# Kernel optimization log

Measured on AMD Instinct MI355X. Metric: run time of the kernel, lower is better.

## Reference

```python
import jax, jax.numpy as jnp
import numpy as np

EPS = 1e-5      # F.layer_norm default eps
ALPHA = 0.08    # ALALLaDA blend coefficient


def setup_inputs() -> dict:
    key = jax.random.key(0)
    ks = jax.random.split(key, 6)
    B, S, D, K = 2, 2048, 2048, 8
    Fh = D // 4
    h_L = jax.random.normal(ks[0], (B, S, D), jnp.float32)
    # nonzero -> masked position (stands in for input_ids == 126336)
    mask = jax.random.randint(ks[1], (B, S), 0, 2).astype(jnp.int32)
    Wr = jax.random.normal(ks[2], (K, D), jnp.float32) / np.sqrt(D).astype(np.float32)
    br = jnp.zeros((K,), jnp.float32)
    W1 = jax.random.normal(ks[3], (K, D, Fh), jnp.float32) / np.sqrt(D).astype(np.float32)
    b1 = jnp.zeros((K, Fh), jnp.float32)
    W2 = jax.random.normal(ks[4], (K, Fh, D), jnp.float32) / np.sqrt(Fh).astype(np.float32)
    b2 = jnp.zeros((K, D), jnp.float32)
    return {"h_L": h_L, "mask": mask, "Wr": Wr, "br": br,
            "W1": W1, "b1": b1, "W2": W2, "b2": b2, "range_r": 8}


def _router_blend(h_L, Wr, br, W1, b1, W2, b2, mask, range_r):
    B, S, D = h_L.shape
    masked = mask != 0
    um = (~masked).astype(h_L.dtype)  # unmasked validity [B,S]
    # Per-token, per-expert outputs M[b,s,k,d]: Linear -> exact GELU -> Linear.
    pre = jnp.einsum('bsd,kdf->bskf', h_L, W1) + b1
    M = jnp.einsum('bskf,kfd->bskd', jax.nn.gelu(pre, approximate=False), W2) + b2
    # Routing weights at every position (softmax over K experts).
    w = jax.nn.softmax(jnp.einsum('bsd,kd->bsk', h_L, Wr) + br, axis=-1)
    # Accumulate weighted expert outputs over the +/-range_r neighbor window,
    # counting only unmasked neighbors. Fixed small loop over 2r offsets.
    num = jnp.zeros((B, S, D), h_L.dtype)
    cnt = jnp.zeros((B, S), h_L.dtype)
    for o in range(-range_r, range_r + 1):
        if o == 0:
            continue
        if o > 0:  # neighbor t = a + o: shift left, zero-pad tail
            Mo = jnp.pad(M[:, o:], ((0, 0), (0, o), (0, 0), (0, 0)))
            vo = jnp.pad(um[:, o:], ((0, 0), (0, o)))
        else:      # neighbor t = a + o (o<0): shift right, zero-pad head
            Mo = jnp.pad(M[:, :o], ((0, 0), (-o, 0), (0, 0), (0, 0)))
            vo = jnp.pad(um[:, :o], ((0, 0), (-o, 0)))
        num = num + vo[..., None] * jnp.einsum('bsk,bskd->bsd', w, Mo)
        cnt = cnt + vo
    has = cnt > 0
    mean = num / jnp.maximum(cnt, 1.0)[..., None]   # mean over valid neighbors
    # layer_norm over d_model, no affine
    mu = mean.mean(-1, keepdims=True)
    var = jnp.mean((mean - mu) ** 2, axis=-1, keepdims=True)
    ln = (mean - mu) / jnp.sqrt(var + EPS)
    # delta is written only at masked positions that had >=1 neighbor
    delta = jnp.where((masked & has)[..., None], ln, 0.0)
    return h_L + ALPHA * delta


def reference(h_L, mask, Wr, br, W1, b1, W2, b2, range_r):
    return _router_blend(h_L, Wr, br, W1, b1, W2, b2, mask, range_r)
```

## Files before the change

### kernel.cpp

```cpp
#include <hip/hip_runtime.h>
#include <hip/hip_bf16.h>
#include <math.h>


#define ALPHA 0.08f
#define EPS 1e-5f

typedef __attribute__((ext_vector_type(8))) __bf16 bf16x8;
typedef __attribute__((ext_vector_type(8))) short short8;
typedef __attribute__((ext_vector_type(4))) float f32x4;

__device__ __forceinline__ unsigned short f2bf(float f) {
  unsigned u = __float_as_uint(f);
  u += 0x7fffu + ((u >> 16) & 1u);
  return (unsigned short)(u >> 16);
}
__device__ __forceinline__ float bf2f(unsigned short b) {
  return __uint_as_float(((unsigned)b) << 16);
}

#define GLD16(gptr, lptr)                                                     \
  __builtin_amdgcn_global_load_lds(                                           \
      (const __attribute__((address_space(1))) void*)(gptr),                  \
      (__attribute__((address_space(3))) void*)(lptr), 16, 0, 0)

#define LD8(p) __builtin_bit_cast(bf16x8, *(const short8*)(p))

__device__ __forceinline__ int wave_incl_scan(int v, int lane) {
#pragma unroll
  for (int off = 1; off < 64; off <<= 1) {
    int t = __shfl_up(v, off);
    if (lane >= off) v += t;
  }
  return v;
}

__global__ __launch_bounds__(256) void prep_kernel(
    const float* __restrict__ h, const int* __restrict__ mask,
    const float* __restrict__ Wr, const float* __restrict__ br,
    const float* __restrict__ W1, const float* __restrict__ W2,
    const int* __restrict__ rptr, float* __restrict__ w,
    unsigned short* __restrict__ hbc, unsigned short* __restrict__ B1t,
    unsigned short* __restrict__ B2t, int* __restrict__ ru,
    int* __restrict__ msk_idx, int* __restrict__ pos2row,
    int* __restrict__ counts) {
  const int bid = blockIdx.x;
  const int tid = threadIdx.x;
  const int lane = tid & 63, wv = tid >> 6;

  if (bid < 16384) {
    __shared__ float tile[32][33];
    int id = bid;
    const float* src;
    unsigned short* dst;
    int C, c0, r0;
    size_t dstStride;
    if (id < 8192) {
      const int k = id >> 10, rem = id & 1023;
      src = W1 + (size_t)k * 2048 * 512;
      dst = B1t + (size_t)k * 512 * 2048;
      C = 512; dstStride = 2048;
      c0 = (rem >> 6) * 32; r0 = (rem & 63) * 32;
    } else {
      id -= 8192;
      const int k = id >> 10, rem = id & 1023;
      src = W2 + (size_t)k * 512 * 2048;
      dst = B2t + (size_t)k * 512;
      C = 2048; dstStride = 4096;
      c0 = (rem >> 4) * 32; r0 = (rem & 15) * 32;
    }
    const int tx = tid & 31, ty = tid >> 5;
#pragma unroll
    for (int i = 0; i < 4; ++i)
      tile[ty + 8 * i][tx] = src[(size_t)(r0 + ty + 8 * i) * C + (c0 + tx)];
    __syncthreads();
#pragma unroll
    for (int i = 0; i < 4; ++i) {
      const int c = c0 + ty + 8 * i;
      dst[(size_t)c * dstStride + (size_t)(r0 + tx)] =
          f2bf(tile[tx][ty + 8 * i]);
    }
    return;
  }

  if (bid < 20480) {
    const int a = bid - 16384;
    const size_t base = (size_t)a * 2048;
    const int d0 = tid * 8;
    float hv[8];
    *(float4*)(hv) = *(const float4*)(h + base + d0);
    *(float4*)(hv + 4) = *(const float4*)(h + base + d0 + 4);
    float acc[8];
#pragma unroll
    for (int k = 0; k < 8; ++k) {
      float wvv[8];
      *(float4*)(wvv) = *(const float4*)(Wr + (size_t)k * 2048 + d0);
      *(float4*)(wvv + 4) = *(const float4*)(Wr + (size_t)k * 2048 + d0 + 4);
      float s = 0.f;
#pragma unroll
      for (int j = 0; j < 8; ++j) s += hv[j] * wvv[j];
      acc[k] = s;
    }
    int c0n = 0;
    {
      const int4* m4p = (const int4*)mask;
#pragma unroll
      for (int q = 0; q < 4; ++q) {
        const int4 v = m4p[tid * 4 + q];
        const int b0 = tid * 16 + q * 4;
        c0n += (v.x == 0 && b0 + 0 < a);
        c0n += (v.y == 0 && b0 + 1 < a);
        c0n += (v.z == 0 && b0 + 2 < a);
        c0n += (v.w == 0 && b0 + 3 < a);
      }
    }
#pragma unroll
    for (int off = 32; off > 0; off >>= 1) {
      c0n += __shfl_down(c0n, off);
#pragma unroll
      for (int k = 0; k < 8; ++k) acc[k] += __shfl_down(acc[k], off);
    }
    __shared__ float red[4][8];
    __shared__ float logits[8];
    __shared__ int rucnt[4];
    __shared__ int rubc;
    if (lane == 0) {
#pragma unroll
      for (int k = 0; k < 8; ++k) red[wv][k] = acc[k];
      rucnt[wv] = c0n;
    }
    __syncthreads();
    if (tid < 8)
      logits[tid] =
          red[0][tid] + red[1][tid] + red[2][tid] + red[3][tid] + br[tid];
    if (tid == 0) rubc = rucnt[0] + rucnt[1] + rucnt[2] + rucnt[3];
    __syncthreads();
    if (tid == 0) {
      float mx = logits[0];
#pragma unroll
      for (int k = 1; k < 8; ++k) mx = fmaxf(mx, logits[k]);
      float e[8], se = 0.f;
#pragma unroll
      for (int k = 0; k < 8; ++k) {
        e[k] = expf(logits[k] - mx);
        se += e[k];
      }
      const float is = 1.f / se;
#pragma unroll
      for (int k = 0; k < 8; ++k) w[(size_t)a * 8 + k] = e[k] * is;
    }
    if (mask[a] == 0) {
      const int i = rubc;
      short8 o;
#pragma unroll
      for (int j = 0; j < 8; ++j) o[j] = (short)f2bf(hv[j]);
      *(short8*)(hbc + (size_t)i * 2048 + d0) = o;
    }
    return;
  }

  {
    __shared__ int sru[4097];
    __shared__ int wsum[4];
    __shared__ int wsum2[4];
    const int t0 = tid * 16;
    int mv[16];
    {
      const int4* p = (const int4*)mask;
#pragma unroll
      for (int q = 0; q < 4; ++q) {
        const int4 v = p[tid * 4 + q];
        mv[q * 4 + 0] = v.x; mv[q * 4 + 1] = v.y;
        mv[q * 4 + 2] = v.z; mv[q * 4 + 3] = v.w;
      }
    }
    int f[16];
    int c = 0;
#pragma unroll
    for (int e = 0; e < 16; ++e) { f[e] = (mv[e] == 0); c += f[e]; }
    const int isc = wave_incl_scan(c, lane);
    if (lane == 63) wsum[wv] = isc;
    __syncthreads();
    if (tid == 0) {
      int accs = 0;
#pragma unroll
      for (int i = 0; i < 4; ++i) { int v = wsum[i]; wsum[i] = accs; accs += v; }
      sru[4096] = accs;
      ru[4096] = accs;
      counts[0] = accs;
    }
    __syncthreads();
    int ex = wsum[wv] + isc - c;
#pragma unroll
    for (int e = 0; e < 16; ++e) {
      sru[t0 + e] = ex;
      ru[t0 + e] = ex;
      ex += f[e];
    }
    __syncthreads();
    const int r = rptr[0];
    int g[16];
    int c2 = 0;
#pragma unroll
    for (int e = 0; e < 16; ++e) {
      const int t = t0 + e;
      const int s = t & 2047, tb = t & ~2047;
      const int lo = max(s - r, 0), hi = min(s + r, 2047);
      const int cnt = sru[tb + hi + 1] - sru[tb + lo];
      g[e] = (mv[e] != 0 && cnt > 0) ? 1 : 0;
      c2 += g[e];
    }
    const int isc2 = wave_incl_scan(c2, lane);
    if (lane == 63) wsum2[wv] = isc2;
    __syncthreads();
    if (tid == 0) {
      int accs = 0;
#pragma unroll
      for (int i = 0; i < 4; ++i) { int v = wsum2[i]; wsum2[i] = accs; accs += v; }
      counts[1] = accs;
    }
    __syncthreads();
    int ex2 = wsum2[wv] + isc2 - c2;
#pragma unroll
    for (int e = 0; e < 16; ++e) {
      const int t = t0 + e;
      pos2row[t] = g[e] ? ex2 : -1;
      if (g[e]) msk_idx[ex2] = t;
      ex2 += g[e];
    }
  }
}

template <int EPI, int BNW>
__global__ __launch_bounds__(512, 2) void gemm_bt_kernel(
    const unsigned short* __restrict__ A, const unsigned short* __restrict__ Bt,
    float* __restrict__ Cf, unsigned short* __restrict__ Cb,
    const float* __restrict__ bias, const int* __restrict__ counts, int cidx,
    int N, int Kd) {
  constexpr int BIW = BNW / 64;
  constexpr int NF = BNW / 32;
  constexpr int SBUF = 16384 + BNW * 64;
  __shared__ __align__(16) unsigned short L[3 * SBUF];
  const int tid = threadIdx.x;
  const int lane = tid & 63;
  const int wid = tid >> 6;
  const int wr = wid >> 1;
  const int wc = wid & 1;
  const int l8 = lane >> 3;
  const int sc = ((lane & 7) ^ l8) * 8;

  const int Mlim = counts[cidx];
  const int nbm = (Mlim + 255) >> 8;
  const int nbn = N / BNW;
  const int ntiles = nbm * nbn;
  const int ntpx = (ntiles + 7) >> 3;
  const int xcd = blockIdx.x & 7;
  const int slot = blockIdx.x >> 3;

  const int arow = (wr * 64 + (lane & 15)) * 64;
  const int brow = 16384 + (wc * (BNW / 2) + (lane & 15)) * 64;
  const int t16 = lane >> 4;
  const int x7 = lane & 7;
  const int s0 = (t16 ^ x7) * 8;
  const int s1 = ((4 + t16) ^ x7) * 8;
  const int nt = Kd >> 6;

#define VMWAIT_P                                                              \
  do {                                                                        \
    if (BIW == 2) asm volatile("s_waitcnt vmcnt(6)" ::: "memory");            \
    else asm volatile("s_waitcnt vmcnt(5)" ::: "memory");                     \
  } while (0)

#define STAGE(buf, t)                                                         \
  {                                                                           \
    const size_t k0_ = (size_t)(t) << 6;                                      \
    unsigned short* la_ = L + (buf) * SBUF + wid * 2048;                      \
    unsigned short* lb_ = L + (buf) * SBUF + 16384 + wid * (512 * BIW);       \
    GLD16(gA + k0_, la_);                                                     \
    GLD16(gA + (size_t)8 * Kd + k0_, la_ + 512);                              \
    GLD16(gA + (size_t)16 * Kd + k0_, la_ + 1024);                            \
    GLD16(gA + (size_t)24 * Kd + k0_, la_ + 1536);                            \
    GLD16(gB + k0_, lb_);                                                     \
    if (BIW == 2) GLD16(gB + (size_t)8 * Kd + k0_, lb_ + 512);                \
  }

#define COMPUTE(buf)                                                          \
  {                                                                           \
    const unsigned short* bb_ = L + (buf) * SBUF;                             \
    bf16x8 a0[4], a1[4], b0[NF], b1[NF];                                      \
    _Pragma("unroll") for (int m = 0; m < 4; ++m) {                           \
      a0[m] = LD8(bb_ + arow + m * 1024 + s0);                                \
      a1[m] = LD8(bb_ + arow + m * 1024 + s1);                                \
    }                                                                         \
    _Pragma("unroll") for (int n = 0; n < NF; ++n) {                          \
      b0[n] = LD8(bb_ + brow + n * 1024 + s0);                                \
      b1[n] = LD8(bb_ + brow + n * 1024 + s1);                                \
    }                                                                         \
    _Pragma("unroll") for (int m = 0; m < 4; ++m)                             \
        _Pragma("unroll") for (int n = 0; n < NF; ++n) {                      \
      acc[m][n] = __builtin_amdgcn_mfma_f32_16x16x32_bf16(a0[m], b0[n],       \
                                                          acc[m][n], 0, 0, 0); \
      acc[m][n] = __builtin_amdgcn_mfma_f32_16x16x32_bf16(a1[m], b1[n],       \
                                                          acc[m][n], 0, 0, 0); \
    }                                                                         \
  }

#pragma unroll 1
  for (int i = slot; i < ntpx; i += 32) {
    const int tau = xcd * ntpx + i;
    if (tau >= ntiles) break;
    const int bn = (tau / nbm) * BNW;
    const int bm = (tau % nbm) * 256;

    f32x4 acc[4][NF];
#pragma unroll
    for (int m = 0; m < 4; ++m)
#pragma unroll
      for (int n = 0; n < NF; ++n) acc[m][n] = (f32x4){0.f, 0.f, 0.f, 0.f};

    const unsigned short* gA = A + (size_t)(bm + wid * 32 + l8) * Kd + sc;
    const unsigned short* gB = Bt + (size_t)(bn + wid * 8 * BIW + l8) * Kd + sc;

    STAGE(0, 0);
    STAGE(1, 1);
    int cb = 0, sb = 2;
#pragma unroll 1
    for (int t = 0; t < nt - 2; ++t) {
      VMWAIT_P;
      __builtin_amdgcn_s_barrier();
      __builtin_amdgcn_sched_barrier(0);
      STAGE(sb, t + 2);
      COMPUTE(cb);
      cb = (cb == 2) ? 0 : cb + 1;
      sb = (sb == 2) ? 0 : sb + 1;
    }
    VMWAIT_P;
    __builtin_amdgcn_s_barrier();
    __builtin_amdgcn_sched_barrier(0);
    COMPUTE(cb);
    cb = (cb == 2) ? 0 : cb + 1;
    asm volatile("s_waitcnt vmcnt(0)" ::: "memory");
    __builtin_amdgcn_s_barrier();
    __builtin_amdgcn_sched_barrier(0);
    COMPUTE(cb);

    const int r0 = bm + wr * 64 + (lane >> 4) * 4;
    const int c0 = bn + wc * (BNW / 2) + (lane & 15);
#pragma unroll
    for (int m = 0; m < 4; ++m) {
#pragma unroll
      for (int n = 0; n < NF; ++n) {
        const int col = c0 + n * 16;
#pragma unroll
        for (int ii = 0; ii < 4; ++ii) {
          const int row = r0 + m * 16 + ii;
          if (row >= Mlim) continue;
          const size_t off = (size_t)row * N + col;
          float v = acc[m][n][ii];
          if (EPI == 1) {
            v += bias[col];
            v = 0.5f * v * (1.0f + erff(v * 0.70710678118654752f));
            Cb[off] = f2bf(v);
          } else {
            Cf[off] = v;
          }
        }
      }
    }
    __builtin_amdgcn_s_barrier();
  }
#undef STAGE
#undef COMPUTE
#undef VMWAIT_P
}

__global__ void window_kernel(const unsigned short* __restrict__ Act_c,
                              const float* __restrict__ w,
                              const int* __restrict__ msk_idx,
                              const int* __restrict__ ru,
                              const int* __restrict__ rptr,
                              const int* __restrict__ counts,
                              unsigned short* __restrict__ G_c) {
  const int Nm = counts[1];
  const int o = blockIdx.y;
  const int q = (Nm + 7) >> 3;
  const int y = o >> 3;
  if (y >= q) return;
  const int i = (o & 7) * q + y;
  if (i >= Nm) return;
  const int a = msk_idx[i];
  const int s = a & 2047;
  const int tb = a & ~2047;
  const int r = rptr[0];
  const int lo = max(s - r, 0), hi = min(s + r, 2047);
  const int jlo = ru[tb + lo], jhi = ru[tb + hi + 1];
  const int c = blockIdx.x * 2048 + threadIdx.x * 8;
  float acc[8] = {0.f, 0.f, 0.f, 0.f, 0.f, 0.f, 0.f, 0.f};
  for (int j = jlo; j < jhi; ++j) {
    const short8 v = *(const short8*)(Act_c + (size_t)j * 4096 + c);
#pragma unroll
    for (int jj = 0; jj < 8; ++jj) acc[jj] += bf2f((unsigned short)v[jj]);
  }
  const float wv = w[(size_t)a * 8 + (c >> 9)];
  short8 o8;
#pragma unroll
  for (int jj = 0; jj < 8; ++jj) o8[jj] = (short)f2bf(acc[jj] * wv);
  *(short8*)(G_c + (size_t)i * 4096 + c) = o8;
}

__global__ void final_kernel(const float* __restrict__ h,
                             const int* __restrict__ pos2row,
                             const float* __restrict__ w,
                             const float* __restrict__ b2,
                             const float* __restrict__ num_c,
                             const int* __restrict__ ru,
                             const int* __restrict__ rptr,
                             float* __restrict__ out) {
  const int a = blockIdx.x;
  const int tid = threadIdx.x;
  const int lane = tid & 63, wid = tid >> 6;
  const size_t base = (size_t)a * 2048;
  const int d0 = tid * 8;
  const int row = pos2row[a];
  if (row < 0) {
    const float4 x0 = *(const float4*)(h + base + d0);
    const float4 x1 = *(const float4*)(h + base + d0 + 4);
    *(float4*)(out + base + d0) = x0;
    *(float4*)(out + base + d0 + 4) = x1;
    return;
  }
  const int s = a & 2047;
  const int tb = a & ~2047;
  const int r = rptr[0];
  const int lo = max(s - r, 0), hi = min(s + r, 2047);
  const int cnt = ru[tb + hi + 1] - ru[tb + lo];
  float wk[8];
#pragma unroll
  for (int k = 0; k < 8; ++k) wk[k] = w[(size_t)a * 8 + k];
  const float cntf = (float)cnt;
  const float icnt = 1.0f / cntf;
  float mval[8];
  float s1 = 0.f, s2 = 0.f;
#pragma unroll
  for (int j = 0; j < 8; ++j) {
    const int d = d0 + j;
    float wb2 = 0.f;
#pragma unroll
    for (int k = 0; k < 8; ++k) wb2 += wk[k] * b2[(size_t)k * 2048 + d];
    const float v = (num_c[(size_t)row * 2048 + d] + cntf * wb2) * icnt;
    mval[j] = v;
    s1 += v;
    s2 += v * v;
  }
#pragma unroll
  for (int off = 32; off > 0; off >>= 1) {
    s1 += __shfl_down(s1, off);
    s2 += __shfl_down(s2, off);
  }
  __shared__ float red[8];
  if (lane == 0) {
    red[wid] = s1;
    red[4 + wid] = s2;
  }
  __syncthreads();
  const float S1 = red[0] + red[1] + red[2] + red[3];
  const float S2 = red[4] + red[5] + red[6] + red[7];
  const float mu = S1 * (1.0f / 2048.0f);
  const float var = S2 * (1.0f / 2048.0f) - mu * mu;
  const float rin = rsqrtf(var + EPS);
#pragma unroll
  for (int j = 0; j < 8; ++j) {
    const int d = d0 + j;
    out[base + d] = h[base + d] + ALPHA * ((mval[j] - mu) * rin);
  }
}

extern "C" void kernel_launch(void* const* d_in, const int* in_sizes, int n_in,
                              void* d_out, int out_size, void* d_ws,
                              size_t ws_size, hipStream_t stream) {
  const float* h = (const float*)d_in[0];
  const int* mask = (const int*)d_in[1];
  const float* Wr = (const float*)d_in[2];
  const float* br = (const float*)d_in[3];
  const float* W1 = (const float*)d_in[4];
  const float* b1 = (const float*)d_in[5];
  const float* W2 = (const float*)d_in[6];
  const float* b2 = (const float*)d_in[7];
  const int* rptr = (const int*)d_in[8];
  float* out = (float*)d_out;

  char* ws = (char*)d_ws;
  unsigned short* hbc = (unsigned short*)(ws + 0);
  unsigned short* B1t = (unsigned short*)(ws + 16777216);
  unsigned short* B2t = (unsigned short*)(ws + 33554432);
  unsigned short* Act_c = (unsigned short*)(ws + 50331648);
  unsigned short* G_c = (unsigned short*)(ws + 83886080);
  float* num_c = (float*)(ws + 50331648);
  float* wbuf = (float*)(ws + 117440512);
  int* ru = (int*)(ws + 117571584);
  int* msk_idx = ru + 4100;
  int* pos2row = msk_idx + 4096;
  int* counts = pos2row + 4096;

  prep_kernel<<<20481, 256, 0, stream>>>(h, mask, Wr, br, W1, W2, rptr, wbuf,
                                         hbc, B1t, B2t, ru, msk_idx, pos2row,
                                         counts);
  gemm_bt_kernel<1, 128><<<256, 512, 0, stream>>>(hbc, B1t, nullptr, Act_c,
                                                  b1, counts, 0, 4096, 2048);
  window_kernel<<<dim3(2, 4096), 256, 0, stream>>>(Act_c, wbuf, msk_idx, ru,
                                                   rptr, counts, G_c);
  gemm_bt_kernel<0, 64><<<256, 512, 0, stream>>>(G_c, B2t, num_c, nullptr,
                                                 nullptr, counts, 1, 2048,
                                                 4096);
  final_kernel<<<4096, 256, 0, stream>>>(h, pos2row, wbuf, b2, num_c, ru,
                                         rptr, out);
}
```

Baseline: 327.2 us.

## Split-K second GEMM, K=32 staging, sliding-window sum in window kernel

The persistent XCD-swizzled GEMM is replaced by a plain 3D grid with K-step 32, a smaller LDS footprint and launch bounds allowing 4 blocks per CU. The second GEMM is split along K into two partial outputs, which the final kernel adds together. The window kernel now walks 32 consecutive positions with a running add/subtract sum over unmasked neighbours, instead of re-summing the whole window for every masked token. The aim is more parallelism for the small second GEMM and less redundant activation reading, at the cost of writing and reading an extra fp32 partial buffer and running more, shorter K loops.

Result: slower. 336.3 us (+2.8%).

```diff
diff --git a/kernel.cpp b/kernel.cpp
--- a/kernel.cpp
+++ b/kernel.cpp
@@ -231,188 +231,181 @@
   }
 }
 
-template <int EPI, int BNW>
-__global__ __launch_bounds__(512, 2) void gemm_bt_kernel(
+template <int EPI>
+__global__ __launch_bounds__(512, 4) void gemm_bt_kernel(
     const unsigned short* __restrict__ A, const unsigned short* __restrict__ Bt,
-    float* __restrict__ Cf, unsigned short* __restrict__ Cb,
-    const float* __restrict__ bias, const int* __restrict__ counts, int cidx,
-    int N, int Kd) {
-  constexpr int BIW = BNW / 64;
-  constexpr int NF = BNW / 32;
-  constexpr int SBUF = 16384 + BNW * 64;
+    float* __restrict__ Cf0, float* __restrict__ Cf1,
+    unsigned short* __restrict__ Cb, const float* __restrict__ bias,
+    const int* __restrict__ counts, int cidx, int N, int Kstride, int Kd) {
+  const int Mlim = counts[cidx];
+  const int bm = blockIdx.y * 256;
+  if (bm >= Mlim) return;
+  const int bn = blockIdx.x * 128;
+  const int kofs = blockIdx.z * Kd;
+  constexpr int SBUF = 12288;
   __shared__ __align__(16) unsigned short L[3 * SBUF];
   const int tid = threadIdx.x;
   const int lane = tid & 63;
   const int wid = tid >> 6;
   const int wr = wid >> 1;
   const int wc = wid & 1;
-  const int l8 = lane >> 3;
-  const int sc = ((lane & 7) ^ l8) * 8;
-
-  const int Mlim = counts[cidx];
-  const int nbm = (Mlim + 255) >> 8;
-  const int nbn = N / BNW;
-  const int ntiles = nbm * nbn;
-  const int ntpx = (ntiles + 7) >> 3;
-  const int xcd = blockIdx.x & 7;
-  const int slot = blockIdx.x >> 3;
-
-  const int arow = (wr * 64 + (lane & 15)) * 64;
-  const int brow = 16384 + (wc * (BNW / 2) + (lane & 15)) * 64;
-  const int t16 = lane >> 4;
-  const int x7 = lane & 7;
-  const int s0 = (t16 ^ x7) * 8;
-  const int s1 = ((4 + t16) ^ x7) * 8;
-  const int nt = Kd >> 6;
-
-#define VMWAIT_P                                                              \
-  do {                                                                        \
-    if (BIW == 2) asm volatile("s_waitcnt vmcnt(6)" ::: "memory");            \
-    else asm volatile("s_waitcnt vmcnt(5)" ::: "memory");                     \
-  } while (0)
+
+  f32x4 acc[4][4];
+#pragma unroll
+  for (int m = 0; m < 4; ++m)
+#pragma unroll
+    for (int n = 0; n < 4; ++n) acc[m][n] = (f32x4){0.f, 0.f, 0.f, 0.f};
+
+  const int l4 = lane >> 2;
+  const int scol = ((lane & 3) ^ (l4 & 3)) * 8;
+  const unsigned short* gA0 =
+      A + (size_t)(bm + wid * 16 + l4) * Kstride + kofs + scol;
+  const unsigned short* gA1 = gA0 + (size_t)128 * Kstride;
+  const unsigned short* gB0 =
+      Bt + (size_t)(bn + wid * 16 + l4) * Kstride + kofs + scol;
+
+  const int swz = ((lane >> 4) ^ (lane & 3)) * 8;
+  const int aoff = (wr * 64 + (lane & 15)) * 32 + swz;
+  const int boff = 8192 + (wc * 64 + (lane & 15)) * 32 + swz;
 
 #define STAGE(buf, t)                                                         \
   {                                                                           \
-    const size_t k0_ = (size_t)(t) << 6;                                      \
-    unsigned short* la_ = L + (buf) * SBUF + wid * 2048;                      \
-    unsigned short* lb_ = L + (buf) * SBUF + 16384 + wid * (512 * BIW);       \
-    GLD16(gA + k0_, la_);                                                     \
-    GLD16(gA + (size_t)8 * Kd + k0_, la_ + 512);                              \
-    GLD16(gA + (size_t)16 * Kd + k0_, la_ + 1024);                            \
-    GLD16(gA + (size_t)24 * Kd + k0_, la_ + 1536);                            \
-    GLD16(gB + k0_, lb_);                                                     \
-    if (BIW == 2) GLD16(gB + (size_t)8 * Kd + k0_, lb_ + 512);                \
+    const int k0_ = (t) << 5;                                                 \
+    unsigned short* la_ = L + (buf) * SBUF + wid * 512;                       \
+    unsigned short* lb_ = L + (buf) * SBUF + 8192 + wid * 512;                \
+    GLD16(gA0 + k0_, la_);                                                    \
+    GLD16(gA1 + k0_, la_ + 4096);                                             \
+    GLD16(gB0 + k0_, lb_);                                                    \
   }
 
 #define COMPUTE(buf)                                                          \
   {                                                                           \
     const unsigned short* bb_ = L + (buf) * SBUF;                             \
-    bf16x8 a0[4], a1[4], b0[NF], b1[NF];                                      \
-    _Pragma("unroll") for (int m = 0; m < 4; ++m) {                           \
-      a0[m] = LD8(bb_ + arow + m * 1024 + s0);                                \
-      a1[m] = LD8(bb_ + arow + m * 1024 + s1);                                \
-    }                                                                         \
-    _Pragma("unroll") for (int n = 0; n < NF; ++n) {                          \
-      b0[n] = LD8(bb_ + brow + n * 1024 + s0);                                \
-      b1[n] = LD8(bb_ + brow + n * 1024 + s1);                                \
-    }                                                                         \
+    bf16x8 af[4], bfr[4];                                                     \
+    _Pragma("unroll") for (int m = 0; m < 4; ++m) af[m] =                     \
+        LD8(bb_ + aoff + m * 512);                                            \
+    _Pragma("unroll") for (int n = 0; n < 4; ++n) bfr[n] =                    \
+        LD8(bb_ + boff + n * 512);                                            \
     _Pragma("unroll") for (int m = 0; m < 4; ++m)                             \
-        _Pragma("unroll") for (int n = 0; n < NF; ++n) {                      \
-      acc[m][n] = __builtin_amdgcn_mfma_f32_16x16x32_bf16(a0[m], b0[n],       \
-                                                          acc[m][n], 0, 0, 0); \
-      acc[m][n] = __builtin_amdgcn_mfma_f32_16x16x32_bf16(a1[m], b1[n],       \
-                                                          acc[m][n], 0, 0, 0); \
-    }                                                                         \
-  }
-
+        _Pragma("unroll") for (int n = 0; n < 4; ++n) acc[m][n] =             \
+            __builtin_amdgcn_mfma_f32_16x16x32_bf16(af[m], bfr[n],            \
+                                                    acc[m][n], 0, 0, 0);      \
+  }
+
+  const int nt = Kd >> 5;
+  STAGE(0, 0);
+  STAGE(1, 1);
+  int cb = 0, sb = 2;
 #pragma unroll 1
-  for (int i = slot; i < ntpx; i += 32) {
-    const int tau = xcd * ntpx + i;
-    if (tau >= ntiles) break;
-    const int bn = (tau / nbm) * BNW;
-    const int bm = (tau % nbm) * 256;
-
-    f32x4 acc[4][NF];
-#pragma unroll
-    for (int m = 0; m < 4; ++m)
-#pragma unroll
-      for (int n = 0; n < NF; ++n) acc[m][n] = (f32x4){0.f, 0.f, 0.f, 0.f};
-
-    const unsigned short* gA = A + (size_t)(bm + wid * 32 + l8) * Kd + sc;
-    const unsigned short* gB = Bt + (size_t)(bn + wid * 8 * BIW + l8) * Kd + sc;
-
-    STAGE(0, 0);
-    STAGE(1, 1);
-    int cb = 0, sb = 2;
-#pragma unroll 1
-    for (int t = 0; t < nt - 2; ++t) {
-      VMWAIT_P;
-      __builtin_amdgcn_s_barrier();
-      __builtin_amdgcn_sched_barrier(0);
-      STAGE(sb, t + 2);
-      COMPUTE(cb);
-      cb = (cb == 2) ? 0 : cb + 1;
-      sb = (sb == 2) ? 0 : sb + 1;
-    }
-    VMWAIT_P;
+  for (int t = 0; t < nt - 2; ++t) {
+    asm volatile("s_waitcnt vmcnt(3)" ::: "memory");
     __builtin_amdgcn_s_barrier();
     __builtin_amdgcn_sched_barrier(0);
+    STAGE(sb, t + 2);
     COMPUTE(cb);
     cb = (cb == 2) ? 0 : cb + 1;
-    asm volatile("s_waitcnt vmcnt(0)" ::: "memory");
-    __builtin_amdgcn_s_barrier();
-    __builtin_amdgcn_sched_barrier(0);
-    COMPUTE(cb);
-
-    const int r0 = bm + wr * 64 + (lane >> 4) * 4;
-    const int c0 = bn + wc * (BNW / 2) + (lane & 15);
-#pragma unroll
-    for (int m = 0; m < 4; ++m) {
-#pragma unroll
-      for (int n = 0; n < NF; ++n) {
-        const int col = c0 + n * 16;
-#pragma unroll
-        for (int ii = 0; ii < 4; ++ii) {
-          const int row = r0 + m * 16 + ii;
-          if (row >= Mlim) continue;
-          const size_t off = (size_t)row * N + col;
-          float v = acc[m][n][ii];
-          if (EPI == 1) {
-            v += bias[col];
-            v = 0.5f * v * (1.0f + erff(v * 0.70710678118654752f));
-            Cb[off] = f2bf(v);
-          } else {
-            Cf[off] = v;
-          }
+    sb = (sb == 2) ? 0 : sb + 1;
+  }
+  asm volatile("s_waitcnt vmcnt(3)" ::: "memory");
+  __builtin_amdgcn_s_barrier();
+  __builtin_amdgcn_sched_barrier(0);
+  COMPUTE(cb);
+  cb = (cb == 2) ? 0 : cb + 1;
+  asm volatile("s_waitcnt vmcnt(0)" ::: "memory");
+  __builtin_amdgcn_s_barrier();
+  __builtin_amdgcn_sched_barrier(0);
+  COMPUTE(cb);
+#undef STAGE
+#undef COMPUTE
+
+  float* __restrict__ Cf = (blockIdx.z == 0) ? Cf0 : Cf1;
+  const int r0 = bm + wr * 64 + (lane >> 4) * 4;
+  const int c0 = bn + wc * 64 + (lane & 15);
+#pragma unroll
+  for (int m = 0; m < 4; ++m) {
+#pragma unroll
+    for (int n = 0; n < 4; ++n) {
+      const int col = c0 + n * 16;
+#pragma unroll
+      for (int ii = 0; ii < 4; ++ii) {
+        const int row = r0 + m * 16 + ii;
+        if (row >= Mlim) continue;
+        const size_t off = (size_t)row * N + col;
+        float v = acc[m][n][ii];
+        if (EPI == 1) {
+          v += bias[col];
+          v = 0.5f * v * (1.0f + erff(v * 0.70710678118654752f));
+          Cb[off] = f2bf(v);
+        } else {
+          Cf[off] = v;
         }
       }
     }
-    __builtin_amdgcn_s_barrier();
-  }
-#undef STAGE
-#undef COMPUTE
-#undef VMWAIT_P
-}
-
-__global__ void window_kernel(const unsigned short* __restrict__ Act_c,
-                              const float* __restrict__ w,
-                              const int* __restrict__ msk_idx,
-                              const int* __restrict__ ru,
-                              const int* __restrict__ rptr,
-                              const int* __restrict__ counts,
-                              unsigned short* __restrict__ G_c) {
-  const int Nm = counts[1];
-  const int o = blockIdx.y;
-  const int q = (Nm + 7) >> 3;
-  const int y = o >> 3;
-  if (y >= q) return;
-  const int i = (o & 7) * q + y;
-  if (i >= Nm) return;
-  const int a = msk_idx[i];
-  const int s = a & 2047;
-  const int tb = a & ~2047;
+  }
+}
+
+__global__ __launch_bounds__(64) void window_kernel(
+    const unsigned short* __restrict__ Act_c, const float* __restrict__ w,
+    const int* __restrict__ ru, const int* __restrict__ pos2row,
+    const int* __restrict__ rptr, unsigned short* __restrict__ G_c) {
+  const int tid = threadIdx.x;
+  const int b = blockIdx.y >> 6;
+  const int seg = blockIdx.y & 63;
+  const int s0 = seg * 32;
+  const int tb = b * 2048;
+  const int cbase = blockIdx.x * 512 + tid * 8;
+  const int kx = cbase >> 9;
   const int r = rptr[0];
-  const int lo = max(s - r, 0), hi = min(s + r, 2047);
-  const int jlo = ru[tb + lo], jhi = ru[tb + hi + 1];
-  const int c = blockIdx.x * 2048 + threadIdx.x * 8;
-  float acc[8] = {0.f, 0.f, 0.f, 0.f, 0.f, 0.f, 0.f, 0.f};
-  for (int j = jlo; j < jhi; ++j) {
-    const short8 v = *(const short8*)(Act_c + (size_t)j * 4096 + c);
-#pragma unroll
-    for (int jj = 0; jj < 8; ++jj) acc[jj] += bf2f((unsigned short)v[jj]);
-  }
-  const float wv = w[(size_t)a * 8 + (c >> 9)];
-  short8 o8;
-#pragma unroll
-  for (int jj = 0; jj < 8; ++jj) o8[jj] = (short)f2bf(acc[jj] * wv);
-  *(short8*)(G_c + (size_t)i * 4096 + c) = o8;
+
+  float W[8] = {0.f, 0.f, 0.f, 0.f, 0.f, 0.f, 0.f, 0.f};
+  for (int t = s0 - r; t <= s0 + r; ++t) {
+    if (t < 0 || t > 2047) continue;
+    const int j = ru[tb + t];
+    if (ru[tb + t + 1] > j) {
+      const short8 v = *(const short8*)(Act_c + (size_t)j * 4096 + cbase);
+#pragma unroll
+      for (int e = 0; e < 8; ++e) W[e] += bf2f((unsigned short)v[e]);
+    }
+  }
+#pragma unroll 1
+  for (int i = 0; i < 32; ++i) {
+    const int t = s0 + i;
+    const int a = tb + t;
+    const int rowo = pos2row[a];
+    if (rowo >= 0) {
+      const float wv = w[(size_t)a * 8 + kx];
+      short8 o8;
+#pragma unroll
+      for (int e = 0; e < 8; ++e) o8[e] = (short)f2bf(W[e] * wv);
+      *(short8*)(G_c + (size_t)rowo * 4096 + cbase) = o8;
+    }
+    const int tin = t + r + 1;
+    if (tin < 2048) {
+      const int j = ru[tb + tin];
+      if (ru[tb + tin + 1] > j) {
+        const short8 v = *(const short8*)(Act_c + (size_t)j * 4096 + cbase);
+#pragma unroll
+        for (int e = 0; e < 8; ++e) W[e] += bf2f((unsigned short)v[e]);
+      }
+    }
+    const int tout = t - r;
+    if (tout >= 0) {
+      const int j = ru[tb + tout];
+      if (ru[tb + tout + 1] > j) {
+        const short8 v = *(const short8*)(Act_c + (size_t)j * 4096 + cbase);
+#pragma unroll
+        for (int e = 0; e < 8; ++e) W[e] -= bf2f((unsigned short)v[e]);
+      }
+    }
+  }
 }
 
 __global__ void final_kernel(const float* __restrict__ h,
                              const int* __restrict__ pos2row,
                              const float* __restrict__ w,
                              const float* __restrict__ b2,
-                             const float* __restrict__ num_c,
+                             const float* __restrict__ p0,
+                             const float* __restrict__ p1,
                              const int* __restrict__ ru,
                              const int* __restrict__ rptr,
                              float* __restrict__ out) {
@@ -447,7 +440,8 @@
     float wb2 = 0.f;
 #pragma unroll
     for (int k = 0; k < 8; ++k) wb2 += wk[k] * b2[(size_t)k * 2048 + d];
-    const float v = (num_c[(size_t)row * 2048 + d] + cntf * wb2) * icnt;
+    const size_t po = (size_t)row * 2048 + d;
+    const float v = (p0[po] + p1[po] + cntf * wb2) * icnt;
     mval[j] = v;
     s1 += v;
     s2 += v * v;
@@ -495,7 +489,8 @@
   unsigned short* B2t = (unsigned short*)(ws + 33554432);
   unsigned short* Act_c = (unsigned short*)(ws + 50331648);
   unsigned short* G_c = (unsigned short*)(ws + 83886080);
-  float* num_c = (float*)(ws + 50331648);
+  float* p0 = (float*)(ws + 50331648);
+  float* p1 = (float*)(ws + 0);
   float* wbuf = (float*)(ws + 117440512);
   int* ru = (int*)(ws + 117571584);
   int* msk_idx = ru + 4100;
@@ -505,13 +500,12 @@
   prep_kernel<<<20481, 256, 0, stream>>>(h, mask, Wr, br, W1, W2, rptr, wbuf,
                                          hbc, B1t, B2t, ru, msk_idx, pos2row,
                                          counts);
-  gemm_bt_kernel<1, 128><<<256, 512, 0, stream>>>(hbc, B1t, nullptr, Act_c,
-                                                  b1, counts, 0, 4096, 2048);
-  window_kernel<<<dim3(2, 4096), 256, 0, stream>>>(Act_c, wbuf, msk_idx, ru,
-                                                   rptr, counts, G_c);
-  gemm_bt_kernel<0, 64><<<256, 512, 0, stream>>>(G_c, B2t, num_c, nullptr,
-                                                 nullptr, counts, 1, 2048,
-                                                 4096);
-  final_kernel<<<4096, 256, 0, stream>>>(h, pos2row, wbuf, b2, num_c, ru,
+  gemm_bt_kernel<1><<<dim3(32, 16, 1), 512, 0, stream>>>(
+      hbc, B1t, nullptr, nullptr, Act_c, b1, counts, 0, 4096, 2048, 2048);
+  window_kernel<<<dim3(8, 128), 64, 0, stream>>>(Act_c, wbuf, ru, pos2row,
+                                                 rptr, G_c);
+  gemm_bt_kernel<0><<<dim3(16, 16, 2), 512, 0, stream>>>(
+      G_c, B2t, p0, p1, nullptr, nullptr, counts, 1, 2048, 4096, 2048);
+  final_kernel<<<4096, 256, 0, stream>>>(h, pos2row, wbuf, b2, p0, p1, ru,
                                          rptr, out);
 }
```
